# Optimization experiments

Hardware: AMD Instinct MI355X
Metric: run time of the kernel (lower is better)

Reference implementation:

```python
import jax, jax.numpy as jnp
import numpy as np

B, N, D = 8, 2048, 256
BIG = 1e9  # max_int_value used to mask the diagonal
LN_EPS = 1e-5  # F.layer_norm default eps


def setup_inputs() -> dict:
    key = jax.random.key(0)
    kq, kk = jax.random.split(key)
    q = jax.random.normal(kq, (B, N, D), dtype=jnp.float32)
    k = jax.random.normal(kk, (B, N, D), dtype=jnp.float32)
    return {"q": q, "k": k, "top_k_instances": 100, "top_k_relationships": 5}


def _forward(q, k, K, R):
    b, n, d = q.shape
    # dense QK^T + softmax over keys -> (b, n, n)
    scores1 = jax.nn.softmax(jnp.einsum('bid,bjd->bij', q, k), axis=-1)
    # instance selection: top-K of the softmaxed diagonal, sorted ascending
    diag = jnp.diagonal(scores1, axis1=-2, axis2=-1)           # (b, n)
    top_idx = jnp.sort(jax.lax.top_k(diag, K)[1], axis=-1)      # (b, K)
    # gather selected rows then selected columns -> (b, K, K)
    sel = jnp.take_along_axis(scores1, top_idx[:, :, None], axis=1)   # (b, K, n)
    rel = jnp.take_along_axis(sel, jnp.broadcast_to(top_idx[:, None, :], (b, K, K)), axis=2)
    # mask diagonal with BIG (masked_fill_ with eye)
    rel = jnp.where(jnp.eye(K, dtype=bool)[None], BIG, rel)
    # top-R relationships per selected instance; torch recovers them via
    # scatter(-1)+where, which yields row-major order with ascending column
    # indices inside each row -> equivalent to sorting top-k indices per row.
    rel_idx = jnp.sort(jax.lax.top_k(rel, R)[1], axis=-1)       # (b, K, R)
    rows = jnp.broadcast_to(jnp.arange(K)[:, None], (K, R)).reshape(-1)  # (K*R,)
    subj = top_idx[:, rows]                                     # (b, K*R) original subject ids
    obj = jnp.take_along_axis(top_idx, rel_idx.reshape(b, K * R), axis=-1)  # (b, K*R)
    batch_ids = jnp.broadcast_to(jnp.arange(b)[:, None], (b, K * R))
    soi = jnp.stack([batch_ids, subj, obj], axis=-1)            # (b, K*R, 3)
    # gather embeddings from q and layer-norm (no affine)
    se = jnp.take_along_axis(q, subj[:, :, None], axis=1)       # (b, K*R, d)
    oe = jnp.take_along_axis(q, obj[:, :, None], axis=1)
    re = se + oe
    mu = jnp.mean(re, axis=-1, keepdims=True)
    var = jnp.var(re, axis=-1, keepdims=True)
    re = (re - mu) * jax.lax.rsqrt(var + LN_EPS)
    return scores1, soi, re


def reference(q, k, top_k_instances, top_k_relationships):
    return _forward(q, k, top_k_instances, top_k_relationships)
```

## Files before the change

kernel.cpp:

```cpp
#include <hip/hip_runtime.h>
#include <math.h>

#define BB 8
#define NN 2048
#define DD 256
#define KK 100
#define RR 5
#define BIGV 1000000000.0f
#define LN_EPS 1e-5f

typedef __attribute__((ext_vector_type(8))) short short8;
typedef __attribute__((ext_vector_type(4))) float floatx4;

__device__ static inline unsigned short f2bf_rne(float x) {
  unsigned int u = __float_as_uint(x);
  unsigned int r = (u + 0x7FFFu + ((u >> 16) & 1u)) >> 16;
  return (unsigned short)r;
}
__device__ static inline float bf2f(unsigned short h) {
  return __uint_as_float(((unsigned int)h) << 16);
}

__device__ static inline void gl_lds16(const unsigned short* g, unsigned short* l) {
  __builtin_amdgcn_global_load_lds(
      (const __attribute__((address_space(1))) unsigned int*)(g),
      (__attribute__((address_space(3))) unsigned int*)(l), 16, 0, 0);
}

__global__ __launch_bounds__(256) void split_bf16(const float* __restrict__ q,
                                                  const float* __restrict__ k,
                                                  ushort4* __restrict__ qhi,
                                                  ushort4* __restrict__ qlo,
                                                  ushort4* __restrict__ khi,
                                                  ushort4* __restrict__ klo) {
  const int n4 = BB * NN * DD / 4;
  const float4* src = (blockIdx.y == 0) ? (const float4*)q : (const float4*)k;
  ushort4* hi = blockIdx.y ? khi : qhi;
  ushort4* lo = blockIdx.y ? klo : qlo;
  for (int i = blockIdx.x * 256 + threadIdx.x; i < n4; i += gridDim.x * 256) {
    float4 v = src[i];
    ushort4 h, l;
    h.x = f2bf_rne(v.x); l.x = f2bf_rne(v.x - bf2f(h.x));
    h.y = f2bf_rne(v.y); l.y = f2bf_rne(v.y - bf2f(h.y));
    h.z = f2bf_rne(v.z); l.z = f2bf_rne(v.z - bf2f(h.z));
    h.w = f2bf_rne(v.w); l.w = f2bf_rne(v.w - bf2f(h.w));
    hi[i] = h; lo[i] = l;
  }
}

__global__ __launch_bounds__(256) void gemm_mfma_split(
    const unsigned short* __restrict__ qhi, const unsigned short* __restrict__ qlo,
    const unsigned short* __restrict__ khi, const unsigned short* __restrict__ klo,
    float* __restrict__ s) {
  __shared__ unsigned short lds[4][8][512];
  const int b = blockIdx.z;
  const int i0 = blockIdx.y * 128, j0 = blockIdx.x * 128;
  const int t = threadIdx.x;
  const int w = t >> 6, L = t & 63;
  const int wx = w & 1, wy = w >> 1;
  const int q_ = L >> 4, m_ = L & 15;

  const size_t bofs = (size_t)b * NN * DD;
  const unsigned short* base;
  {
    const unsigned short* bases0 = qhi + bofs;
    const unsigned short* bases1 = qlo + bofs;
    const unsigned short* bases2 = khi + bofs;
    const unsigned short* bases3 = klo + bofs;
    base = (w == 0) ? bases0 : (w == 1) ? bases1 : (w == 2) ? bases2 : bases3;
  }
  const int rowbase = (w < 2 ? i0 : j0);

  floatx4 acc[4][4];
#pragma unroll
  for (int i = 0; i < 4; ++i)
#pragma unroll
    for (int j = 0; j < 4; ++j) acc[i][j] = (floatx4){0.f, 0.f, 0.f, 0.f};

  for (int kb0 = 0; kb0 < DD; kb0 += 32) {
#pragma unroll
    for (int r = 0; r < 8; ++r) {
      const unsigned short* gp =
          base + (size_t)(rowbase + r * 16 + m_) * DD + kb0 + q_ * 8;
      gl_lds16(gp, &lds[w][r][0]);
    }
    __syncthreads();

    short8 ah[4], al[4], bh[4], bl[4];
#pragma unroll
    for (int i = 0; i < 4; ++i) {
      ah[i] = *(const short8*)&lds[0][wy * 4 + i][L * 8];
      al[i] = *(const short8*)&lds[1][wy * 4 + i][L * 8];
      bh[i] = *(const short8*)&lds[2][wx * 4 + i][L * 8];
      bl[i] = *(const short8*)&lds[3][wx * 4 + i][L * 8];
    }
#pragma unroll
    for (int i = 0; i < 4; ++i)
#pragma unroll
      for (int j = 0; j < 4; ++j) {
        acc[i][j] = __builtin_amdgcn_mfma_f32_16x16x32_bf16(ah[i], bh[j], acc[i][j], 0, 0, 0);
        acc[i][j] = __builtin_amdgcn_mfma_f32_16x16x32_bf16(ah[i], bl[j], acc[i][j], 0, 0, 0);
        acc[i][j] = __builtin_amdgcn_mfma_f32_16x16x32_bf16(al[i], bh[j], acc[i][j], 0, 0, 0);
      }
    __syncthreads();
  }

#pragma unroll
  for (int i = 0; i < 4; ++i)
#pragma unroll
    for (int j = 0; j < 4; ++j)
#pragma unroll
      for (int r = 0; r < 4; ++r) {
        int row = i0 + wy * 64 + i * 16 + q_ * 4 + r;
        int col = j0 + wx * 64 + j * 16 + m_;
        s[((size_t)b * NN + row) * NN + col] = acc[i][j][r];
      }
}

__global__ __launch_bounds__(256) void gemm_logits(const float* __restrict__ q,
                                                   const float* __restrict__ k,
                                                   float* __restrict__ s) {
  __shared__ float As[32][132];
  __shared__ float Bs[32][132];
  const int b = blockIdx.z;
  const int i0 = blockIdx.y * 128;
  const int j0 = blockIdx.x * 128;
  const int t = threadIdx.x;
  const int tx = t & 15;
  const int ty = t >> 4;
  const float* qb = q + (size_t)b * NN * DD;
  const float* kb = k + (size_t)b * NN * DD;

  float acc[8][8];
#pragma unroll
  for (int i = 0; i < 8; ++i)
#pragma unroll
    for (int j = 0; j < 8; ++j) acc[i][j] = 0.f;

  for (int kb0 = 0; kb0 < DD; kb0 += 32) {
#pragma unroll
    for (int l = 0; l < 4; ++l) {
      int f = l * 256 + t;
      int row = f >> 3;
      int c4 = (f & 7) * 4;
      float4 va = *(const float4*)(qb + (size_t)(i0 + row) * DD + kb0 + c4);
      float4 vb = *(const float4*)(kb + (size_t)(j0 + row) * DD + kb0 + c4);
      As[c4 + 0][row] = va.x; As[c4 + 1][row] = va.y;
      As[c4 + 2][row] = va.z; As[c4 + 3][row] = va.w;
      Bs[c4 + 0][row] = vb.x; Bs[c4 + 1][row] = vb.y;
      Bs[c4 + 2][row] = vb.z; Bs[c4 + 3][row] = vb.w;
    }
    __syncthreads();
#pragma unroll
    for (int kk = 0; kk < 32; ++kk) {
      float a[8], bv[8];
      *(float4*)&a[0] = *(const float4*)&As[kk][ty * 8];
      *(float4*)&a[4] = *(const float4*)&As[kk][ty * 8 + 4];
      *(float4*)&bv[0] = *(const float4*)&Bs[kk][tx * 8];
      *(float4*)&bv[4] = *(const float4*)&Bs[kk][tx * 8 + 4];
#pragma unroll
      for (int i = 0; i < 8; ++i)
#pragma unroll
        for (int j = 0; j < 8; ++j) acc[i][j] += a[i] * bv[j];
    }
    __syncthreads();
  }

#pragma unroll
  for (int i = 0; i < 8; ++i) {
    size_t row = (size_t)(i0 + ty * 8 + i);
    float* po = s + ((size_t)b * NN + row) * NN + j0 + tx * 8;
    *(float4*)po = make_float4(acc[i][0], acc[i][1], acc[i][2], acc[i][3]);
    *(float4*)(po + 4) = make_float4(acc[i][4], acc[i][5], acc[i][6], acc[i][7]);
  }
}

__device__ inline float pick4(float4 v, int j) {
  return j == 0 ? v.x : (j == 1 ? v.y : (j == 2 ? v.z : v.w));
}

__global__ __launch_bounds__(256) void softmax_rows(float* __restrict__ s,
                                                    float* __restrict__ diag) {
  const int bi = blockIdx.x;
  const int irow = bi & (NN - 1);
  const int t = threadIdx.x;
  float4* rowp = (float4*)(s + (size_t)bi * NN);
  float4 v0 = rowp[t];
  float4 v1 = rowp[256 + t];

  __shared__ float red[4];
  float m = fmaxf(fmaxf(fmaxf(v0.x, v0.y), fmaxf(v0.z, v0.w)),
                  fmaxf(fmaxf(v1.x, v1.y), fmaxf(v1.z, v1.w)));
#pragma unroll
  for (int off = 32; off; off >>= 1) m = fmaxf(m, __shfl_xor(m, off));
  if ((t & 63) == 0) red[t >> 6] = m;
  __syncthreads();
  m = fmaxf(fmaxf(red[0], red[1]), fmaxf(red[2], red[3]));
  __syncthreads();

  float4 e0, e1;
  e0.x = expf(v0.x - m); e0.y = expf(v0.y - m);
  e0.z = expf(v0.z - m); e0.w = expf(v0.w - m);
  e1.x = expf(v1.x - m); e1.y = expf(v1.y - m);
  e1.z = expf(v1.z - m); e1.w = expf(v1.w - m);
  float sum = e0.x + e0.y + e0.z + e0.w + e1.x + e1.y + e1.z + e1.w;
#pragma unroll
  for (int off = 32; off; off >>= 1) sum += __shfl_xor(sum, off);
  if ((t & 63) == 0) red[t >> 6] = sum;
  __syncthreads();
  sum = red[0] + red[1] + red[2] + red[3];

  float inv = 1.0f / sum;
  float4 s0 = make_float4(e0.x * inv, e0.y * inv, e0.z * inv, e0.w * inv);
  float4 s1 = make_float4(e1.x * inv, e1.y * inv, e1.z * inv, e1.w * inv);
  rowp[t] = s0;
  rowp[256 + t] = s1;

  int c0 = t * 4;
  if (irow >= c0 && irow < c0 + 4) diag[bi] = pick4(s0, irow - c0);
  int c1 = 1024 + t * 4;
  if (irow >= c1 && irow < c1 + 4) diag[bi] = pick4(s1, irow - c1);
}

__global__ __launch_bounds__(1024) void topk_diag(const float* __restrict__ diag,
                                                  int* __restrict__ topidx) {
  const int b = blockIdx.x;
  const int t = threadIdx.x;
  __shared__ unsigned long long key[NN];
  __shared__ int idxs[KK];

#pragma unroll
  for (int sIt = 0; sIt < 2; ++sIt) {
    int i = t + sIt * 1024;
    unsigned int vb = __float_as_uint(diag[b * NN + i]);
    key[i] = ((unsigned long long)vb << 32) | (unsigned int)(NN - 1 - i);
  }
  __syncthreads();

  for (int kstep = 2; kstep <= NN; kstep <<= 1) {
    for (int j = kstep >> 1; j > 0; j >>= 1) {
      int i = ((t & ~(j - 1)) << 1) | (t & (j - 1));
      int l = i | j;
      unsigned long long a = key[i];
      unsigned long long c = key[l];
      bool desc = ((i & kstep) == 0);
      if (desc ? (a < c) : (a > c)) { key[i] = c; key[l] = a; }
      __syncthreads();
    }
  }

  if (t < KK) idxs[t] = NN - 1 - (int)(unsigned int)(key[t] & 0xFFFFFFFFu);
  __syncthreads();
  if (t < KK) {
    int myidx = idxs[t];
    int rank = 0;
#pragma unroll 4
    for (int j = 0; j < KK; ++j) rank += (idxs[j] < myidx) ? 1 : 0;
    topidx[b * KK + rank] = myidx;
  }
}

__global__ __launch_bounds__(256) void rel_topk(const float* __restrict__ s,
                                                const int* __restrict__ topidx,
                                                float* __restrict__ soi,
                                                int2* __restrict__ pairs) {
  const int b = blockIdx.x;
  const int t = threadIdx.x;
  __shared__ int tix[KK];
  __shared__ float rel[KK][KK + 1];
  if (t < KK) tix[t] = topidx[b * KK + t];
  __syncthreads();

  for (int e = t; e < KK * KK; e += 256) {
    int i = e / KK;
    int j = e - i * KK;
    rel[i][j] = (i == j) ? BIGV : s[((size_t)b * NN + tix[i]) * NN + tix[j]];
  }
  __syncthreads();

  if (t < KK) {
    int sel[RR];
#pragma unroll
    for (int r = 0; r < RR; ++r) sel[r] = -1;
#pragma unroll
    for (int r = 0; r < RR; ++r) {
      float best = -2.f;
      int bj = -1;
      for (int j = 0; j < KK; ++j) {
        bool taken = false;
#pragma unroll
        for (int sN = 0; sN < RR; ++sN)
          if (sN < r && sel[sN] == j) taken = true;
        if (taken) continue;
        float v = rel[t][j];
        if (v > best) { best = v; bj = j; }
      }
      sel[r] = bj;
    }
#pragma unroll
    for (int a2 = 0; a2 < RR; ++a2)
#pragma unroll
      for (int b2 = a2 + 1; b2 < RR; ++b2)
        if (sel[b2] < sel[a2]) { int tmp = sel[a2]; sel[a2] = sel[b2]; sel[b2] = tmp; }

    int subj = tix[t];
#pragma unroll
    for (int r = 0; r < RR; ++r) {
      int obj = tix[sel[r]];
      size_t p = ((size_t)b * KK + t) * RR + r;
      soi[p * 3 + 0] = (float)b;
      soi[p * 3 + 1] = (float)subj;
      soi[p * 3 + 2] = (float)obj;
      pairs[p] = make_int2(subj, obj);
    }
  }
}

__global__ __launch_bounds__(64) void edge_ln(const float* __restrict__ q,
                                              const int2* __restrict__ pairs,
                                              float* __restrict__ re) {
  const int p = blockIdx.x;
  const int b = p / (KK * RR);
  const int l = threadIdx.x;
  int2 pr = pairs[p];
  const float4* qs = (const float4*)(q + ((size_t)b * NN + pr.x) * DD);
  const float4* qo = (const float4*)(q + ((size_t)b * NN + pr.y) * DD);
  float4 a = qs[l];
  float4 o = qo[l];
  a.x += o.x; a.y += o.y; a.z += o.z; a.w += o.w;
  float sum = a.x + a.y + a.z + a.w;
  float sq = a.x * a.x + a.y * a.y + a.z * a.z + a.w * a.w;
#pragma unroll
  for (int off = 32; off; off >>= 1) {
    sum += __shfl_xor(sum, off);
    sq += __shfl_xor(sq, off);
  }
  float mu = sum * (1.f / DD);
  float var = sq * (1.f / DD) - mu * mu;
  float rs = rsqrtf(var + LN_EPS);
  float4 r4 = make_float4((a.x - mu) * rs, (a.y - mu) * rs,
                          (a.z - mu) * rs, (a.w - mu) * rs);
  ((float4*)(re + (size_t)p * DD))[l] = r4;
}

extern "C" void kernel_launch(void* const* d_in, const int* in_sizes, int n_in,
                              void* d_out, int out_size, void* d_ws, size_t ws_size,
                              hipStream_t stream) {
  const float* q = (const float*)d_in[0];
  const float* k = (const float*)d_in[1];

  float* out = (float*)d_out;
  float* scores = out;
  float* soi = out + (size_t)BB * NN * NN;
  float* re = soi + (size_t)BB * KK * RR * 3;

  char* ws = (char*)d_ws;
  float* diag = (float*)ws;
  int* topidx = (int*)(ws + (size_t)BB * NN * 4);
  int2* pairs = (int2*)(ws + (size_t)BB * NN * 4 + (size_t)BB * KK * 4);
  const size_t small_end = 128 * 1024;
  const size_t plane = (size_t)BB * NN * DD * 2;
  const bool use_mfma = ws_size >= small_end + 4 * plane;

  if (use_mfma) {
    unsigned short* qhi = (unsigned short*)(ws + small_end);
    unsigned short* qlo = (unsigned short*)(ws + small_end + plane);
    unsigned short* khi = (unsigned short*)(ws + small_end + 2 * plane);
    unsigned short* klo = (unsigned short*)(ws + small_end + 3 * plane);
    split_bf16<<<dim3(1024, 2), 256, 0, stream>>>(q, k, (ushort4*)qhi, (ushort4*)qlo,
                                                  (ushort4*)khi, (ushort4*)klo);
    gemm_mfma_split<<<dim3(NN / 128, NN / 128, BB), 256, 0, stream>>>(qhi, qlo, khi, klo,
                                                                      scores);
  } else {
    gemm_logits<<<dim3(NN / 128, NN / 128, BB), 256, 0, stream>>>(q, k, scores);
  }
  softmax_rows<<<dim3(BB * NN), 256, 0, stream>>>(scores, diag);
  topk_diag<<<dim3(BB), 1024, 0, stream>>>(diag, topidx);
  rel_topk<<<dim3(BB), 256, 0, stream>>>(scores, topidx, soi, pairs);
  edge_ln<<<dim3(BB * KK * RR), 64, 0, stream>>>(q, pairs, re);
}
```

Baseline: 326.7 us.

## Fuse split-bf16 GEMM with row softmax, keeping full rows in registers

Result: slower. 699.6 us (+114.1%).

```diff
diff --git a/kernel.cpp b/kernel.cpp
--- a/kernel.cpp
+++ b/kernel.cpp
@@ -48,73 +48,134 @@
   }
 }
 
-__global__ __launch_bounds__(256) void gemm_mfma_split(
+__global__ __launch_bounds__(512) void gemm_softmax(
     const unsigned short* __restrict__ qhi, const unsigned short* __restrict__ qlo,
     const unsigned short* __restrict__ khi, const unsigned short* __restrict__ klo,
     float* __restrict__ s) {
-  __shared__ unsigned short lds[4][8][512];
-  const int b = blockIdx.z;
-  const int i0 = blockIdx.y * 128, j0 = blockIdx.x * 128;
+  __shared__ unsigned short ldsA[2][2][512];
+  __shared__ unsigned short ldsB[16][2][512];
+  __shared__ float red[2][16][4];
+
   const int t = threadIdx.x;
   const int w = t >> 6, L = t & 63;
-  const int wx = w & 1, wy = w >> 1;
+  const int wy = w & 1, wg = w >> 1;
   const int q_ = L >> 4, m_ = L & 15;
+  const int b = blockIdx.x & 7;
+  const int i0 = (blockIdx.x >> 3) * 32;
 
   const size_t bofs = (size_t)b * NN * DD;
-  const unsigned short* base;
-  {
-    const unsigned short* bases0 = qhi + bofs;
-    const unsigned short* bases1 = qlo + bofs;
-    const unsigned short* bases2 = khi + bofs;
-    const unsigned short* bases3 = klo + bofs;
-    base = (w == 0) ? bases0 : (w == 1) ? bases1 : (w == 2) ? bases2 : bases3;
-  }
-  const int rowbase = (w < 2 ? i0 : j0);
-
-  floatx4 acc[4][4];
-#pragma unroll
-  for (int i = 0; i < 4; ++i)
-#pragma unroll
-    for (int j = 0; j < 4; ++j) acc[i][j] = (floatx4){0.f, 0.f, 0.f, 0.f};
-
-  for (int kb0 = 0; kb0 < DD; kb0 += 32) {
-#pragma unroll
-    for (int r = 0; r < 8; ++r) {
-      const unsigned short* gp =
-          base + (size_t)(rowbase + r * 16 + m_) * DD + kb0 + q_ * 8;
-      gl_lds16(gp, &lds[w][r][0]);
-    }
-    __syncthreads();
-
-    short8 ah[4], al[4], bh[4], bl[4];
+  const unsigned short* qh = qhi + bofs;
+  const unsigned short* ql = qlo + bofs;
+  const unsigned short* kh = khi + bofs;
+  const unsigned short* kl = klo + bofs;
+
+  floatx4 acc[32];
+#pragma unroll
+  for (int i = 0; i < 32; ++i) acc[i] = (floatx4){0.f, 0.f, 0.f, 0.f};
+
+  for (int ch = 0; ch < 8; ++ch) {
+    const int c0 = ch * 256;
+    for (int ks = 0; ks < 8; ++ks) {
+      const int kb0 = ks * 32;
+#pragma unroll
+      for (int r = 0; r < 5; ++r) {
+        int T = w + 8 * r;
+        if (T < 36) {
+          const unsigned short* gp;
+          unsigned short* dst;
+          if (T < 4) {
+            int a = T >> 1, p = T & 1;
+            const unsigned short* base = p ? ql : qh;
+            gp = base + (size_t)(i0 + a * 16 + m_) * DD + kb0 + q_ * 8;
+            dst = &ldsA[a][p][0];
+          } else {
+            int Tb = T - 4;
+            int c = Tb >> 1, p = Tb & 1;
+            const unsigned short* base = p ? kl : kh;
+            gp = base + (size_t)(c0 + c * 16 + m_) * DD + kb0 + q_ * 8;
+            dst = &ldsB[c][p][0];
+          }
+          gl_lds16(gp, dst);
+        }
+      }
+      __syncthreads();
+
+      short8 ah = *(const short8*)&ldsA[wy][0][L * 8];
+      short8 al = *(const short8*)&ldsA[wy][1][L * 8];
+#pragma unroll
+      for (int i = 0; i < 4; ++i) {
+        int c = wg * 4 + i;
+        short8 bh = *(const short8*)&ldsB[c][0][L * 8];
+        short8 bl = *(const short8*)&ldsB[c][1][L * 8];
+        int ai = ch * 4 + i;
+        acc[ai] = __builtin_amdgcn_mfma_f32_16x16x32_bf16(ah, bh, acc[ai], 0, 0, 0);
+        acc[ai] = __builtin_amdgcn_mfma_f32_16x16x32_bf16(ah, bl, acc[ai], 0, 0, 0);
+        acc[ai] = __builtin_amdgcn_mfma_f32_16x16x32_bf16(al, bh, acc[ai], 0, 0, 0);
+      }
+      __syncthreads();
+    }
+  }
+
+  float rmax[4];
+#pragma unroll
+  for (int r = 0; r < 4; ++r) {
+    float m = -3.4e38f;
+#pragma unroll
+    for (int i = 0; i < 32; ++i) m = fmaxf(m, acc[i][r]);
+    rmax[r] = m;
+  }
+#pragma unroll
+  for (int off = 8; off; off >>= 1)
+#pragma unroll
+    for (int r = 0; r < 4; ++r) rmax[r] = fmaxf(rmax[r], __shfl_xor(rmax[r], off));
+  if (m_ == 0)
+#pragma unroll
+    for (int r = 0; r < 4; ++r) red[wy][q_ * 4 + r][wg] = rmax[r];
+  __syncthreads();
+  float M[4];
+#pragma unroll
+  for (int r = 0; r < 4; ++r) {
+    int ri = q_ * 4 + r;
+    M[r] = fmaxf(fmaxf(red[wy][ri][0], red[wy][ri][1]),
+                 fmaxf(red[wy][ri][2], red[wy][ri][3]));
+  }
+  __syncthreads();
+
+  float rsum[4] = {0.f, 0.f, 0.f, 0.f};
+#pragma unroll
+  for (int i = 0; i < 32; ++i)
+#pragma unroll
+    for (int r = 0; r < 4; ++r) {
+      float e = expf(acc[i][r] - M[r]);
+      acc[i][r] = e;
+      rsum[r] += e;
+    }
+#pragma unroll
+  for (int off = 8; off; off >>= 1)
+#pragma unroll
+    for (int r = 0; r < 4; ++r) rsum[r] += __shfl_xor(rsum[r], off);
+  if (m_ == 0)
+#pragma unroll
+    for (int r = 0; r < 4; ++r) red[wy][q_ * 4 + r][wg] = rsum[r];
+  __syncthreads();
+  float inv[4];
+#pragma unroll
+  for (int r = 0; r < 4; ++r) {
+    int ri = q_ * 4 + r;
+    inv[r] = 1.0f / (red[wy][ri][0] + red[wy][ri][1] + red[wy][ri][2] + red[wy][ri][3]);
+  }
+
+#pragma unroll
+  for (int ch = 0; ch < 8; ++ch)
 #pragma unroll
     for (int i = 0; i < 4; ++i) {
-      ah[i] = *(const short8*)&lds[0][wy * 4 + i][L * 8];
-      al[i] = *(const short8*)&lds[1][wy * 4 + i][L * 8];
-      bh[i] = *(const short8*)&lds[2][wx * 4 + i][L * 8];
-      bl[i] = *(const short8*)&lds[3][wx * 4 + i][L * 8];
-    }
-#pragma unroll
-    for (int i = 0; i < 4; ++i)
-#pragma unroll
-      for (int j = 0; j < 4; ++j) {
-        acc[i][j] = __builtin_amdgcn_mfma_f32_16x16x32_bf16(ah[i], bh[j], acc[i][j], 0, 0, 0);
-        acc[i][j] = __builtin_amdgcn_mfma_f32_16x16x32_bf16(ah[i], bl[j], acc[i][j], 0, 0, 0);
-        acc[i][j] = __builtin_amdgcn_mfma_f32_16x16x32_bf16(al[i], bh[j], acc[i][j], 0, 0, 0);
+      int col = (ch * 16 + wg * 4 + i) * 16 + m_;
+#pragma unroll
+      for (int r = 0; r < 4; ++r) {
+        int row = i0 + wy * 16 + q_ * 4 + r;
+        s[((size_t)b * NN + row) * NN + col] = acc[ch * 4 + i][r] * inv[r];
       }
-    __syncthreads();
-  }
-
-#pragma unroll
-  for (int i = 0; i < 4; ++i)
-#pragma unroll
-    for (int j = 0; j < 4; ++j)
-#pragma unroll
-      for (int r = 0; r < 4; ++r) {
-        int row = i0 + wy * 64 + i * 16 + q_ * 4 + r;
-        int col = j0 + wx * 64 + j * 16 + m_;
-        s[((size_t)b * NN + row) * NN + col] = acc[i][j][r];
-      }
+    }
 }
 
 __global__ __launch_bounds__(256) void gemm_logits(const float* __restrict__ q,
@@ -175,14 +236,8 @@
   }
 }
 
-__device__ inline float pick4(float4 v, int j) {
-  return j == 0 ? v.x : (j == 1 ? v.y : (j == 2 ? v.z : v.w));
-}
-
-__global__ __launch_bounds__(256) void softmax_rows(float* __restrict__ s,
-                                                    float* __restrict__ diag) {
+__global__ __launch_bounds__(256) void softmax_rows(float* __restrict__ s) {
   const int bi = blockIdx.x;
-  const int irow = bi & (NN - 1);
   const int t = threadIdx.x;
   float4* rowp = (float4*)(s + (size_t)bi * NN);
   float4 v0 = rowp[t];
@@ -211,18 +266,11 @@
   sum = red[0] + red[1] + red[2] + red[3];
 
   float inv = 1.0f / sum;
-  float4 s0 = make_float4(e0.x * inv, e0.y * inv, e0.z * inv, e0.w * inv);
-  float4 s1 = make_float4(e1.x * inv, e1.y * inv, e1.z * inv, e1.w * inv);
-  rowp[t] = s0;
-  rowp[256 + t] = s1;
-
-  int c0 = t * 4;
-  if (irow >= c0 && irow < c0 + 4) diag[bi] = pick4(s0, irow - c0);
-  int c1 = 1024 + t * 4;
-  if (irow >= c1 && irow < c1 + 4) diag[bi] = pick4(s1, irow - c1);
-}
-
-__global__ __launch_bounds__(1024) void topk_diag(const float* __restrict__ diag,
+  rowp[t] = make_float4(e0.x * inv, e0.y * inv, e0.z * inv, e0.w * inv);
+  rowp[256 + t] = make_float4(e1.x * inv, e1.y * inv, e1.z * inv, e1.w * inv);
+}
+
+__global__ __launch_bounds__(1024) void topk_diag(const float* __restrict__ s,
                                                   int* __restrict__ topidx) {
   const int b = blockIdx.x;
   const int t = threadIdx.x;
@@ -232,7 +280,7 @@
 #pragma unroll
   for (int sIt = 0; sIt < 2; ++sIt) {
     int i = t + sIt * 1024;
-    unsigned int vb = __float_as_uint(diag[b * NN + i]);
+    unsigned int vb = __float_as_uint(s[((size_t)b * NN + i) * NN + i]);
     key[i] = ((unsigned long long)vb << 32) | (unsigned int)(NN - 1 - i);
   }
   __syncthreads();
@@ -355,9 +403,8 @@
   float* re = soi + (size_t)BB * KK * RR * 3;
 
   char* ws = (char*)d_ws;
-  float* diag = (float*)ws;
-  int* topidx = (int*)(ws + (size_t)BB * NN * 4);
-  int2* pairs = (int2*)(ws + (size_t)BB * NN * 4 + (size_t)BB * KK * 4);
+  int* topidx = (int*)ws;
+  int2* pairs = (int2*)(ws + 64 * 1024);
   const size_t small_end = 128 * 1024;
   const size_t plane = (size_t)BB * NN * DD * 2;
   const bool use_mfma = ws_size >= small_end + 4 * plane;
@@ -369,13 +416,12 @@
     unsigned short* klo = (unsigned short*)(ws + small_end + 3 * plane);
     split_bf16<<<dim3(1024, 2), 256, 0, stream>>>(q, k, (ushort4*)qhi, (ushort4*)qlo,
                                                   (ushort4*)khi, (ushort4*)klo);
-    gemm_mfma_split<<<dim3(NN / 128, NN / 128, BB), 256, 0, stream>>>(qhi, qlo, khi, klo,
-                                                                      scores);
+    gemm_softmax<<<dim3(BB * NN / 32), 512, 0, stream>>>(qhi, qlo, khi, klo, scores);
   } else {
     gemm_logits<<<dim3(NN / 128, NN / 128, BB), 256, 0, stream>>>(q, k, scores);
-  }
-  softmax_rows<<<dim3(BB * NN), 256, 0, stream>>>(scores, diag);
-  topk_diag<<<dim3(BB), 1024, 0, stream>>>(diag, topidx);
+    softmax_rows<<<dim3(BB * NN), 256, 0, stream>>>(scores);
+  }
+  topk_diag<<<dim3(BB), 1024, 0, stream>>>(scores, topidx);
   rel_topk<<<dim3(BB), 256, 0, stream>>>(scores, topidx, soi, pairs);
   edge_ln<<<dim3(BB * KK * RR), 64, 0, stream>>>(q, pairs, re);
 }
```
